# Optimization experiments

Measured on AMD Instinct MI355X. Metric: run time of the kernel, lower is better.

Reference implementation:

```python
import jax, jax.numpy as jnp
import numpy as np

T = 40           # rollout steps
ATT_TEMP = 5.0   # Arbiter attention temperature
ACT_CLIP = 3.5


def setup_inputs() -> dict:
    key = jax.random.key(0)
    ks = jax.random.split(key, 6)
    B, D = 262144, 128
    # states: vel >= 0, dx > 0 (dx is a divisor)
    unscaled_s = jax.random.uniform(ks[0], (B, T, 7), dtype=jnp.float32)
    unscaled_s = unscaled_s.at[:, :, 0].set(unscaled_s[:, :, 0] * 20.0 + 5.0)   # vel
    unscaled_s = unscaled_s.at[:, :, 2].set(unscaled_s[:, :, 2] * 4.0 - 2.0)    # dv (leader)
    unscaled_s = unscaled_s.at[:, :, 3].set(unscaled_s[:, :, 3] * 50.0 + 10.0)  # dx (leader)
    unscaled_s = unscaled_s.at[:, :, 5].set(unscaled_s[:, :, 5] * 4.0 - 2.0)    # dv (merger)
    unscaled_s = unscaled_s.at[:, :, 6].set(unscaled_s[:, :, 6] * 50.0 + 10.0)  # dx (merger)
    # idm params: all strictly positive (sqrt + division)
    p = jax.random.uniform(ks[1], (B, 5), dtype=jnp.float32)
    idm_param = jnp.stack([
        p[:, 0] * 10.0 + 20.0,  # desired_v
        p[:, 1] * 1.0 + 0.5,    # desired_tgap
        p[:, 2] * 3.0 + 1.0,    # min_jamx
        p[:, 3] * 2.0 + 0.5,    # max_act
        p[:, 4] * 2.0 + 0.5,    # min_act
    ], axis=1)
    decoder_output = jax.random.normal(ks[2], (B, D), dtype=jnp.float32)
    W1 = jax.random.normal(ks[3], (D, 100), dtype=jnp.float32) * 0.05
    b1 = jnp.zeros((100,), dtype=jnp.float32)
    W2 = jax.random.normal(ks[4], (100, T), dtype=jnp.float32) * 0.05
    b2 = jnp.zeros((T,), dtype=jnp.float32)
    return {"unscaled_s": unscaled_s, "idm_param": idm_param,
            "decoder_output": decoder_output, "W1": W1, "b1": b1, "W2": W2, "b2": b2}


def _idm_driver(vel, dv, dx, idm_param):
    # vel/dv/dx: [B, T, 1]; idm_param: [B, 5]
    p = idm_param[:, None, :]  # [B, 1, 5]
    desired_v, desired_tgap, min_jamx, max_act, min_act = (
        p[..., 0:1], p[..., 1:2], p[..., 2:3], p[..., 3:4], p[..., 4:5])
    desired_gap = min_jamx + desired_tgap * vel + vel * dv / (2.0 * jnp.sqrt(max_act * min_act))
    act = max_act * (1.0 - (vel / desired_v) ** 4 - (desired_gap / dx) ** 2)
    return jnp.clip(act, -ACT_CLIP, ACT_CLIP)


def reference(unscaled_s, idm_param, decoder_output, W1, b1, W2, b2):
    B = unscaled_s.shape[0]
    # The 40-step loop has no cross-step dependency -> fully vectorized over T.
    s = unscaled_s[:, :T, :]                 # [B, T, 7]
    vel = s[:, :, 0:1]
    fl_seq = _idm_driver(vel, s[:, :, 2:3], s[:, :, 3:4], idm_param)  # [B, T, 1]
    fm_seq = _idm_driver(vel, s[:, :, 5:6], s[:, :, 6:7], idm_param)  # [B, T, 1]
    # Arbiter: two dense layers + temperature sigmoid
    h = decoder_output @ W1 + b1
    logits = h @ W2 + b2                      # [B, T]
    att_scores = jax.nn.sigmoid(ATT_TEMP * logits).reshape(B, T, 1)
    act_seq = att_scores * fl_seq + (1.0 - att_scores) * fm_seq
    return act_seq, att_scores
```

## Files before the change

kernel.cpp:

```cpp
#include <hip/hip_runtime.h>


#define TT 40
#define DD 128
#define ACT_CLIP 3.5f
#define ATT_TEMP 5.0f

typedef short short8 __attribute__((ext_vector_type(8)));
typedef float f32x4 __attribute__((ext_vector_type(4)));

__device__ __forceinline__ unsigned int bf16_rne(float v) {
    unsigned int u = __float_as_uint(v);
    return (u + 0x7FFFu + ((u >> 16) & 1u)) >> 16;
}

__global__ __launch_bounds__(256) void precompute_pack(
    const float* __restrict__ W1, const float* __restrict__ b1,
    const float* __restrict__ W2, const float* __restrict__ b2,
    unsigned int* __restrict__ wpack,
    float* __restrict__ bcp)
{
    int idx = blockIdx.x * 256 + threadIdx.x;
    if (idx < 1536) {
        int l   = idx & 63;
        int rec = idx >> 6;
        int h   = rec & 1;
        int sn  = rec >> 1;
        int n   = sn % 3, s = sn / 3;
        int col = n * 16 + (l & 15);
        int k0  = s * 32 + (l >> 4) * 8;
        unsigned short hv[8];
#pragma unroll
        for (int j = 0; j < 8; ++j) {
            float v = 0.0f;
            if (col < TT) {
                int k = k0 + j;
                for (int m = 0; m < 100; ++m)
                    v = fmaf(W1[k * 100 + m], W2[m * TT + col], v);
            }
            unsigned int hi = bf16_rne(v);
            float hif = __uint_as_float(hi << 16);
            unsigned int lo = bf16_rne(v - hif);
            hv[j] = (unsigned short)(h == 0 ? hi : lo);
        }
        uint4 o;
        o.x = hv[0] | ((unsigned)hv[1] << 16);
        o.y = hv[2] | ((unsigned)hv[3] << 16);
        o.z = hv[4] | ((unsigned)hv[5] << 16);
        o.w = hv[6] | ((unsigned)hv[7] << 16);
        reinterpret_cast<uint4*>(wpack)[idx] = o;
    } else if (idx < 1536 + 48) {
        int t = idx - 1536;
        float v = 0.0f;
        if (t < TT) {
            v = b2[t];
            for (int m = 0; m < 100; ++m)
                v = fmaf(b1[m], W2[m * TT + t], v);
        }
        bcp[t] = v;
    }
}

__global__ __launch_bounds__(256, 4) void matvec_att(
    const float* __restrict__ x,
    const unsigned int* __restrict__ wpack,
    const float* __restrict__ bcp,
    float* __restrict__ attout)
{
    __shared__ unsigned int swp[6144];
    __shared__ float sbc[48];
    __shared__ float satt[64 * TT];

    int tid = threadIdx.x;
    {
        const uint4* src = reinterpret_cast<const uint4*>(wpack);
        uint4* dst = reinterpret_cast<uint4*>(swp);
#pragma unroll
        for (int i = 0; i < 6; ++i) dst[tid + 256 * i] = src[tid + 256 * i];
        if (tid < 48) sbc[tid] = bcp[tid];
    }
    __syncthreads();

    int wave = tid >> 6, lane = tid & 63;
    int l15 = lane & 15, lk = lane >> 4;
    size_t row0 = (size_t)blockIdx.x * 64 + wave * 16 + l15;
    const float* xr = x + row0 * DD;

    float4 xv[8];
#pragma unroll
    for (int s = 0; s < 4; ++s) {
        xv[2 * s]     = *reinterpret_cast<const float4*>(xr + s * 32 + lk * 8);
        xv[2 * s + 1] = *reinterpret_cast<const float4*>(xr + s * 32 + lk * 8 + 4);
    }

    f32x4 acc[3] = {f32x4{0,0,0,0}, f32x4{0,0,0,0}, f32x4{0,0,0,0}};

#pragma unroll
    for (int s = 0; s < 4; ++s) {
        float fs[8] = {xv[2*s].x, xv[2*s].y, xv[2*s].z, xv[2*s].w,
                       xv[2*s+1].x, xv[2*s+1].y, xv[2*s+1].z, xv[2*s+1].w};
        union { unsigned int u[4]; short8 v; } ah, al;
#pragma unroll
        for (int p = 0; p < 4; ++p) {
            unsigned int h0 = bf16_rne(fs[2*p]);
            unsigned int h1 = bf16_rne(fs[2*p+1]);
            float f0 = __uint_as_float(h0 << 16);
            float f1 = __uint_as_float(h1 << 16);
            unsigned int l0 = bf16_rne(fs[2*p] - f0);
            unsigned int l1 = bf16_rne(fs[2*p+1] - f1);
            ah.u[p] = h0 | (h1 << 16);
            al.u[p] = l0 | (l1 << 16);
        }
#pragma unroll
        for (int n = 0; n < 3; ++n) {
            int base = (s * 3 + n) * 512;
            short8 bh = *reinterpret_cast<const short8*>(&swp[base + lane * 4]);
            short8 bl = *reinterpret_cast<const short8*>(&swp[base + 256 + lane * 4]);
            acc[n] = __builtin_amdgcn_mfma_f32_16x16x32_bf16(ah.v, bh, acc[n], 0, 0, 0);
            acc[n] = __builtin_amdgcn_mfma_f32_16x16x32_bf16(al.v, bh, acc[n], 0, 0, 0);
            acc[n] = __builtin_amdgcn_mfma_f32_16x16x32_bf16(ah.v, bl, acc[n], 0, 0, 0);
        }
    }

#pragma unroll
    for (int n = 0; n < 3; ++n) {
        int col = n * 16 + l15;
        if (col < TT) {
            float bias = sbc[col];
#pragma unroll
            for (int r = 0; r < 4; ++r) {
                int rowl = wave * 16 + lk * 4 + r;
                float L = acc[n][r] + bias;
                satt[rowl * TT + col] =
                    __builtin_amdgcn_rcpf(1.0f + __expf(-ATT_TEMP * L));
            }
        }
    }
    __syncthreads();

    float4* dst = reinterpret_cast<float4*>(attout + (size_t)blockIdx.x * 64 * TT);
    const float4* s4 = reinterpret_cast<const float4*>(satt);
    for (int i = tid; i < 640; i += 256) dst[i] = s4[i];
}

__global__ __launch_bounds__(320, 8) void epilogue_k(
    const float* __restrict__ us, const float* __restrict__ prm,
    const float* __restrict__ attg,
    float* __restrict__ act)
{
    unsigned int t0 = blockIdx.x * 320u + threadIdx.x;

    const float4* fv = reinterpret_cast<const float4*>(us) + t0 * 7u;
    float f[28];
#pragma unroll
    for (int q = 0; q < 7; ++q) {
        float4 v = fv[q];
        f[q * 4 + 0] = v.x; f[q * 4 + 1] = v.y;
        f[q * 4 + 2] = v.z; f[q * 4 + 3] = v.w;
    }
    float4 a4 = reinterpret_cast<const float4*>(attg)[t0];
    float av[4] = {a4.x, a4.y, a4.z, a4.w};

    unsigned int row_g = t0 / 10u;
    const float* pr = prm + (size_t)row_g * 5u;
    float desired_v    = pr[0];
    float desired_tgap = pr[1];
    float min_jamx     = pr[2];
    float max_act      = pr[3];
    float min_act      = pr[4];
    float inv_dv = __builtin_amdgcn_rcpf(desired_v);
    float coef   = 0.5f / sqrtf(max_act * min_act);

    float ares[4];
#pragma unroll
    for (int tt = 0; tt < 4; ++tt) {
        float vel = f[tt * 7 + 0];
        float dvl = f[tt * 7 + 2], dxl = f[tt * 7 + 3];
        float dvm = f[tt * 7 + 5], dxm = f[tt * 7 + 6];

        float r  = vel * inv_dv;
        float r2 = r * r;
        float common = 1.0f - r2 * r2;
        float base = fmaf(desired_tgap, vel, min_jamx);
        float gl = fmaf(vel * dvl, coef, base);
        float gm = fmaf(vel * dvm, coef, base);
        float ql = gl * __builtin_amdgcn_rcpf(dxl);
        float qm = gm * __builtin_amdgcn_rcpf(dxm);
        float al = max_act * (common - ql * ql);
        float am = max_act * (common - qm * qm);
        al = fminf(fmaxf(al, -ACT_CLIP), ACT_CLIP);
        am = fminf(fmaxf(am, -ACT_CLIP), ACT_CLIP);
        ares[tt] = fmaf(av[tt], al - am, am);
    }
    reinterpret_cast<float4*>(act)[t0] =
        make_float4(ares[0], ares[1], ares[2], ares[3]);
}

extern "C" void kernel_launch(void* const* d_in, const int* in_sizes, int n_in,
                              void* d_out, int out_size, void* d_ws, size_t ws_size,
                              hipStream_t stream) {
    const float* us  = (const float*)d_in[0];
    const float* prm = (const float*)d_in[1];
    const float* x   = (const float*)d_in[2];
    const float* W1  = (const float*)d_in[3];
    const float* b1  = (const float*)d_in[4];
    const float* W2  = (const float*)d_in[5];
    const float* b2  = (const float*)d_in[6];
    float* out = (float*)d_out;

    int B = in_sizes[1] / 5;

    unsigned int* wpack = (unsigned int*)d_ws;
    float* bcp = (float*)((char*)d_ws + 24576);

    float* attout = out + (size_t)B * TT;

    hipLaunchKernelGGL(precompute_pack, dim3(7), dim3(256), 0, stream,
                       W1, b1, W2, b2, wpack, bcp);
    hipLaunchKernelGGL(matvec_att, dim3(B / 64), dim3(256), 0, stream,
                       x, wpack, bcp, attout);
    hipLaunchKernelGGL(epilogue_k, dim3(B / 32), dim3(320), 0, stream,
                       us, prm, attout, out);
}
```

Before: 137.5 us.

## Read packed weights from global, truncate bf16 split, nontemporal epilogue I/O

The matvec kernel stops staging the 24KB packed weight and bias tables into shared memory and reads them directly from global/L2 per MFMA step. This drops the per-block copy and barrier and raises the occupancy hint. The hi/lo bf16 split of x switches from round-to-nearest to truncation, which is cheaper but may slightly change accuracy. The epilogue moves to 256-thread blocks and uses nontemporal loads and stores on the streamed state and output. The matvec output copy is also unrolled.

```diff
diff --git a/kernel.cpp b/kernel.cpp
--- a/kernel.cpp
+++ b/kernel.cpp
@@ -61,29 +61,19 @@
     }
 }
 
-__global__ __launch_bounds__(256, 4) void matvec_att(
+__global__ __launch_bounds__(256, 6) void matvec_att(
     const float* __restrict__ x,
     const unsigned int* __restrict__ wpack,
     const float* __restrict__ bcp,
     float* __restrict__ attout)
 {
-    __shared__ unsigned int swp[6144];
-    __shared__ float sbc[48];
     __shared__ float satt[64 * TT];
 
     int tid = threadIdx.x;
-    {
-        const uint4* src = reinterpret_cast<const uint4*>(wpack);
-        uint4* dst = reinterpret_cast<uint4*>(swp);
-#pragma unroll
-        for (int i = 0; i < 6; ++i) dst[tid + 256 * i] = src[tid + 256 * i];
-        if (tid < 48) sbc[tid] = bcp[tid];
-    }
-    __syncthreads();
-
     int wave = tid >> 6, lane = tid & 63;
     int l15 = lane & 15, lk = lane >> 4;
-    size_t row0 = (size_t)blockIdx.x * 64 + wave * 16 + l15;
+    size_t blk = blockIdx.x;
+    size_t row0 = blk * 64 + wave * 16 + l15;
     const float* xr = x + row0 * DD;
 
     float4 xv[8];
@@ -102,20 +92,19 @@
         union { unsigned int u[4]; short8 v; } ah, al;
 #pragma unroll
         for (int p = 0; p < 4; ++p) {
-            unsigned int h0 = bf16_rne(fs[2*p]);
-            unsigned int h1 = bf16_rne(fs[2*p+1]);
-            float f0 = __uint_as_float(h0 << 16);
-            float f1 = __uint_as_float(h1 << 16);
-            unsigned int l0 = bf16_rne(fs[2*p] - f0);
-            unsigned int l1 = bf16_rne(fs[2*p+1] - f1);
-            ah.u[p] = h0 | (h1 << 16);
-            al.u[p] = l0 | (l1 << 16);
+            unsigned int u0 = __float_as_uint(fs[2*p]);
+            unsigned int u1 = __float_as_uint(fs[2*p+1]);
+            ah.u[p] = (u0 >> 16) | (u1 & 0xFFFF0000u);
+            float r0 = fs[2*p]   - __uint_as_float(u0 & 0xFFFF0000u);
+            float r1 = fs[2*p+1] - __uint_as_float(u1 & 0xFFFF0000u);
+            al.u[p] = (__float_as_uint(r0) >> 16) |
+                      (__float_as_uint(r1) & 0xFFFF0000u);
         }
 #pragma unroll
         for (int n = 0; n < 3; ++n) {
             int base = (s * 3 + n) * 512;
-            short8 bh = *reinterpret_cast<const short8*>(&swp[base + lane * 4]);
-            short8 bl = *reinterpret_cast<const short8*>(&swp[base + 256 + lane * 4]);
+            short8 bh = *reinterpret_cast<const short8*>(&wpack[base + lane * 4]);
+            short8 bl = *reinterpret_cast<const short8*>(&wpack[base + 256 + lane * 4]);
             acc[n] = __builtin_amdgcn_mfma_f32_16x16x32_bf16(ah.v, bh, acc[n], 0, 0, 0);
             acc[n] = __builtin_amdgcn_mfma_f32_16x16x32_bf16(al.v, bh, acc[n], 0, 0, 0);
             acc[n] = __builtin_amdgcn_mfma_f32_16x16x32_bf16(ah.v, bl, acc[n], 0, 0, 0);
@@ -126,7 +115,7 @@
     for (int n = 0; n < 3; ++n) {
         int col = n * 16 + l15;
         if (col < TT) {
-            float bias = sbc[col];
+            float bias = bcp[col];
 #pragma unroll
             for (int r = 0; r < 4; ++r) {
                 int rowl = wave * 16 + lk * 4 + r;
@@ -138,28 +127,19 @@
     }
     __syncthreads();
 
-    float4* dst = reinterpret_cast<float4*>(attout + (size_t)blockIdx.x * 64 * TT);
+    float4* dst = reinterpret_cast<float4*>(attout + blk * 64 * TT);
     const float4* s4 = reinterpret_cast<const float4*>(satt);
-    for (int i = tid; i < 640; i += 256) dst[i] = s4[i];
-}
-
-__global__ __launch_bounds__(320, 8) void epilogue_k(
+    dst[tid]       = s4[tid];
+    dst[tid + 256] = s4[tid + 256];
+    if (tid < 128) dst[tid + 512] = s4[tid + 512];
+}
+
+__global__ __launch_bounds__(256, 6) void epilogue_k(
     const float* __restrict__ us, const float* __restrict__ prm,
     const float* __restrict__ attg,
     float* __restrict__ act)
 {
-    unsigned int t0 = blockIdx.x * 320u + threadIdx.x;
-
-    const float4* fv = reinterpret_cast<const float4*>(us) + t0 * 7u;
-    float f[28];
-#pragma unroll
-    for (int q = 0; q < 7; ++q) {
-        float4 v = fv[q];
-        f[q * 4 + 0] = v.x; f[q * 4 + 1] = v.y;
-        f[q * 4 + 2] = v.z; f[q * 4 + 3] = v.w;
-    }
-    float4 a4 = reinterpret_cast<const float4*>(attg)[t0];
-    float av[4] = {a4.x, a4.y, a4.z, a4.w};
+    unsigned int t0 = blockIdx.x * 256u + threadIdx.x;
 
     unsigned int row_g = t0 / 10u;
     const float* pr = prm + (size_t)row_g * 5u;
@@ -168,6 +148,23 @@
     float min_jamx     = pr[2];
     float max_act      = pr[3];
     float min_act      = pr[4];
+
+    const f32x4* fv = reinterpret_cast<const f32x4*>(us) + t0 * 7u;
+    f32x4 v0 = __builtin_nontemporal_load(fv + 0);
+    f32x4 v1 = __builtin_nontemporal_load(fv + 1);
+    f32x4 v2 = __builtin_nontemporal_load(fv + 2);
+    f32x4 v3 = __builtin_nontemporal_load(fv + 3);
+    f32x4 v4 = __builtin_nontemporal_load(fv + 4);
+    f32x4 v5 = __builtin_nontemporal_load(fv + 5);
+    f32x4 v6 = __builtin_nontemporal_load(fv + 6);
+    f32x4 a4 = reinterpret_cast<const f32x4*>(attg)[t0];
+
+    float f[28] = {v0.x, v0.y, v0.z, v0.w, v1.x, v1.y, v1.z, v1.w,
+                   v2.x, v2.y, v2.z, v2.w, v3.x, v3.y, v3.z, v3.w,
+                   v4.x, v4.y, v4.z, v4.w, v5.x, v5.y, v5.z, v5.w,
+                   v6.x, v6.y, v6.z, v6.w};
+    float av[4] = {a4.x, a4.y, a4.z, a4.w};
+
     float inv_dv = __builtin_amdgcn_rcpf(desired_v);
     float coef   = 0.5f / sqrtf(max_act * min_act);
 
@@ -192,8 +189,8 @@
         am = fminf(fmaxf(am, -ACT_CLIP), ACT_CLIP);
         ares[tt] = fmaf(av[tt], al - am, am);
     }
-    reinterpret_cast<float4*>(act)[t0] =
-        make_float4(ares[0], ares[1], ares[2], ares[3]);
+    f32x4 res = {ares[0], ares[1], ares[2], ares[3]};
+    __builtin_nontemporal_store(res, reinterpret_cast<f32x4*>(act) + t0);
 }
 
 extern "C" void kernel_launch(void* const* d_in, const int* in_sizes, int n_in,
@@ -219,6 +216,6 @@
                        W1, b1, W2, b2, wpack, bcp);
     hipLaunchKernelGGL(matvec_att, dim3(B / 64), dim3(256), 0, stream,
                        x, wpack, bcp, attout);
-    hipLaunchKernelGGL(epilogue_k, dim3(B / 32), dim3(320), 0, stream,
+    hipLaunchKernelGGL(epilogue_k, dim3(B * 10 / 256), dim3(256), 0, stream,
                        us, prm, attout, out);
 }
```

Result: slower. 198.4 us (+44.2%).
